# Optimization experiments

Hardware: AMD Instinct MI355X
Metric: run time of the kernel (lower is better)

## Reference

```python
import jax, jax.numpy as jnp
import numpy as np

B, T, D, H = 4, 2048, 1024, 16
Dh = D // H


def setup_inputs() -> dict:
    key = jax.random.key(0)
    ks = jax.random.split(key, 10)
    s = 0.02  # init scale for weights
    return {
        "x": jax.random.normal(ks[0], (B, T, D), jnp.float32),
        "gates": jax.random.uniform(ks[1], (B, H), jnp.float32),
        "Wq": jax.random.normal(ks[2], (D, D), jnp.float32) * s,
        "bq": jnp.zeros((D,), jnp.float32),
        "Wk": jax.random.normal(ks[3], (D, D), jnp.float32) * s,
        "bk": jnp.zeros((D,), jnp.float32),
        "Wv": jax.random.normal(ks[4], (D, D), jnp.float32) * s,
        "bv": jnp.zeros((D,), jnp.float32),
        "Wo": jax.random.normal(ks[5], (D, D), jnp.float32) * s,
        "bo": jnp.zeros((D,), jnp.float32),
    }


def reference(x, gates, Wq, bq, Wk, bk, Wv, bv, Wo, bo):
    # x: [B,T,D], gates: [B,H]. torch Linear is y = x @ W.T + b.
    b, t, d = x.shape
    h = gates.shape[1]
    dh = d // h
    q = (x @ Wq.T + bq).reshape(b, t, h, dh)
    k = (x @ Wk.T + bk).reshape(b, t, h, dh)
    v = (x @ Wv.T + bv).reshape(b, t, h, dh)
    scores = jnp.einsum('bthd,bshd->bhts', q, k) / jnp.sqrt(jnp.float32(dh))
    A = jax.nn.softmax(scores, axis=-1)
    A = A * gates[:, :, None, None]  # post-softmax per-head gate
    z = jnp.einsum('bhts,bshd->bthd', A, v).reshape(b, t, d)
    out = z @ Wo.T + bo
    return out, A
```

## Files before the change

kernel.cpp:

```cpp
#include <hip/hip_runtime.h>

#define BB 4
#define TT 2048
#define DD 1024
#define HH 16
#define DHH 64

using half8  = __attribute__((ext_vector_type(8))) _Float16;
using half4v = __attribute__((ext_vector_type(4))) _Float16;
using f32x4  = __attribute__((ext_vector_type(4))) float;

#define EXP2C 0.18033688011112042f

__device__ __forceinline__ float fexp2(float x) {
#if __has_builtin(__builtin_amdgcn_exp2f)
  return __builtin_amdgcn_exp2f(x);
#else
  return exp2f(x);
#endif
}

__device__ __forceinline__ void gload_lds16(const _Float16* g, _Float16* l) {
  __builtin_amdgcn_global_load_lds((const __attribute__((address_space(1))) void*)g,
                                   (__attribute__((address_space(3))) void*)l, 16, 0, 0);
}

__global__ void cvt_all(const float* __restrict__ x,
                        const float* __restrict__ wq, const float* __restrict__ wk,
                        const float* __restrict__ wv, const float* __restrict__ wo,
                        _Float16* __restrict__ xh,
                        _Float16* __restrict__ wqh, _Float16* __restrict__ wkh,
                        _Float16* __restrict__ wvh, _Float16* __restrict__ woh) {
  const float* s; _Float16* d; int n8, b0, nb;
  int b = blockIdx.x;
  if (b < 512) { s = x; d = xh; n8 = BB * TT * DD / 8; b0 = b; nb = 512; }
  else {
    int wsel = (b - 512) >> 6;
    b0 = (b - 512) & 63; nb = 64; n8 = DD * DD / 8;
    s = wsel == 0 ? wq : wsel == 1 ? wk : wsel == 2 ? wv : wo;
    d = wsel == 0 ? wqh : wsel == 1 ? wkh : wsel == 2 ? wvh : woh;
  }
  for (int i = b0 * 256 + threadIdx.x; i < n8; i += nb * 256) {
    const float4* p = (const float4*)(s + (size_t)i * 8);
    float4 a = p[0], bb = p[1];
    half8 h;
    h[0] = (_Float16)a.x; h[1] = (_Float16)a.y; h[2] = (_Float16)a.z; h[3] = (_Float16)a.w;
    h[4] = (_Float16)bb.x; h[5] = (_Float16)bb.y; h[6] = (_Float16)bb.z; h[7] = (_Float16)bb.w;
    *(half8*)(d + (size_t)i * 8) = h;
  }
}

#define GEMM_STAGE(K0, BSEL)                                                        \
  _Pragma("unroll") for (int it = 0; it < 4; ++it) {                                \
    int chunk = tid + it * 256;                                                     \
    int r = chunk >> 3, pb = chunk & 7, lb = pb ^ (r & 7);                          \
    gload_lds16(A + (size_t)(row0 + r) * K + (K0) * 64 + lb * 8, As[BSEL] + chunk * 8);  \
    gload_lds16(Bw + (size_t)(col0 + r) * K + (K0) * 64 + lb * 8, Bs[BSEL] + chunk * 8); \
  }

__global__ __launch_bounds__(256, 2) void gemm_qkv(const _Float16* __restrict__ A,
                                                   const _Float16* __restrict__ Wqh,
                                                   const _Float16* __restrict__ Wkh,
                                                   const _Float16* __restrict__ Wvh,
                                                   const float* __restrict__ bq,
                                                   const float* __restrict__ bk,
                                                   const float* __restrict__ bv,
                                                   _Float16* __restrict__ qh,
                                                   _Float16* __restrict__ kh,
                                                   _Float16* __restrict__ vTh) {
  constexpr int K = 1024;
  __shared__ _Float16 As[2][128 * 64];
  __shared__ _Float16 Bs[2][128 * 64];
  const int tid = threadIdx.x;
  const int l = tid & 63, w = tid >> 6;
  const int wm = w >> 1, wn = w & 1;
  const int lg = l >> 4, lr16 = l & 15;
  const int wsel = (int)blockIdx.y >> 3;
  const _Float16* Bw = wsel == 0 ? Wqh : wsel == 1 ? Wkh : Wvh;
  const float* bias = wsel == 0 ? bq : wsel == 1 ? bk : bv;
  const int row0 = blockIdx.x * 128, col0 = ((int)blockIdx.y & 7) * 128;

  f32x4 acc[4][4];
#pragma unroll
  for (int i = 0; i < 4; ++i)
#pragma unroll
    for (int j = 0; j < 4; ++j) acc[i][j] = (f32x4)0.0f;

  GEMM_STAGE(0, 0);
  int cur = 0;
  for (int k0 = 0; k0 < 16; ++k0) {
    __syncthreads();
    if (k0 < 15) GEMM_STAGE(k0 + 1, cur ^ 1);
#pragma unroll
    for (int kb = 0; kb < 2; ++kb) {
      half8 a[4], b[4];
#pragma unroll
      for (int f = 0; f < 4; ++f) {
        int ar = wm * 64 + f * 16 + lr16;
        a[f] = *(const half8*)(As[cur] + ar * 64 + ((kb * 4 + lg) ^ (ar & 7)) * 8);
        int br = wn * 64 + f * 16 + lr16;
        b[f] = *(const half8*)(Bs[cur] + br * 64 + ((kb * 4 + lg) ^ (br & 7)) * 8);
      }
#pragma unroll
      for (int i = 0; i < 4; ++i)
#pragma unroll
        for (int j = 0; j < 4; ++j)
          acc[i][j] = __builtin_amdgcn_mfma_f32_16x16x32_f16(a[i], b[j], acc[i][j], 0, 0, 0);
    }
    cur ^= 1;
  }

#pragma unroll
  for (int fi = 0; fi < 4; ++fi) {
#pragma unroll
    for (int fj = 0; fj < 4; ++fj) {
      int gi0 = row0 + wm * 64 + fi * 16 + lg * 4;
      int gj = col0 + wn * 64 + fj * 16 + lr16;
      float bj = bias[gj];
      int b = gi0 >> 11, t0 = gi0 & 2047;
      int h = gj >> 6, dh = gj & 63;
      if (wsel < 2) {
        _Float16* O = wsel ? kh : qh;
#pragma unroll
        for (int r = 0; r < 4; ++r)
          O[(((size_t)(b * HH + h) * TT + (t0 + r)) << 6) + dh] = (_Float16)(acc[fi][fj][r] + bj);
      } else {
        half4v tmp;
#pragma unroll
        for (int r = 0; r < 4; ++r) tmp[r] = (_Float16)(acc[fi][fj][r] + bj);
        *(half4v*)(vTh + (((size_t)(b * HH + h) * DHH + dh) * TT + t0)) = tmp;
      }
    }
  }
}

__global__ __launch_bounds__(256, 2) void gemm_out(const _Float16* __restrict__ A,
                                                   const _Float16* __restrict__ Bw,
                                                   const float* __restrict__ bias,
                                                   float* __restrict__ Cout) {
  constexpr int K = 1024;
  __shared__ _Float16 As[2][128 * 64];
  __shared__ _Float16 Bs[2][128 * 64];
  const int tid = threadIdx.x;
  const int l = tid & 63, w = tid >> 6;
  const int wm = w >> 1, wn = w & 1;
  const int lg = l >> 4, lr16 = l & 15;
  const int row0 = blockIdx.x * 128, col0 = blockIdx.y * 128;

  f32x4 acc[4][4];
#pragma unroll
  for (int i = 0; i < 4; ++i)
#pragma unroll
    for (int j = 0; j < 4; ++j) acc[i][j] = (f32x4)0.0f;

  GEMM_STAGE(0, 0);
  int cur = 0;
  for (int k0 = 0; k0 < 16; ++k0) {
    __syncthreads();
    if (k0 < 15) GEMM_STAGE(k0 + 1, cur ^ 1);
#pragma unroll
    for (int kb = 0; kb < 2; ++kb) {
      half8 a[4], b[4];
#pragma unroll
      for (int f = 0; f < 4; ++f) {
        int ar = wm * 64 + f * 16 + lr16;
        a[f] = *(const half8*)(As[cur] + ar * 64 + ((kb * 4 + lg) ^ (ar & 7)) * 8);
        int br = wn * 64 + f * 16 + lr16;
        b[f] = *(const half8*)(Bs[cur] + br * 64 + ((kb * 4 + lg) ^ (br & 7)) * 8);
      }
#pragma unroll
      for (int i = 0; i < 4; ++i)
#pragma unroll
        for (int j = 0; j < 4; ++j)
          acc[i][j] = __builtin_amdgcn_mfma_f32_16x16x32_f16(a[i], b[j], acc[i][j], 0, 0, 0);
    }
    cur ^= 1;
  }

#pragma unroll
  for (int fi = 0; fi < 4; ++fi) {
#pragma unroll
    for (int fj = 0; fj < 4; ++fj) {
      int gi0 = row0 + wm * 64 + fi * 16 + lg * 4;
      int gj = col0 + wn * 64 + fj * 16 + lr16;
      float bj = bias[gj];
#pragma unroll
      for (int r = 0; r < 4; ++r)
        __builtin_nontemporal_store(acc[fi][fj][r] + bj, &Cout[(size_t)(gi0 + r) * DD + gj]);
    }
  }
}

__global__ __launch_bounds__(512, 2) void attn_kernel(const _Float16* __restrict__ qh,
                                                      const _Float16* __restrict__ kh,
                                                      const _Float16* __restrict__ vTh,
                                                      const float* __restrict__ gates,
                                                      float* __restrict__ Aout,
                                                      _Float16* __restrict__ zh) {
  __shared__ _Float16 Qs[128 * 64];
  __shared__ _Float16 Ks[2][64 * 64];
  __shared__ _Float16 Vs[2][64 * 64];
  __shared__ _Float16 Ps[128 * 64];
  const int tid = threadIdx.x;
  const int l = tid & 63, w = tid >> 6;
  const int lg = l >> 4, lr16 = l & 15;
  const int wr0 = w * 16;
  const int blk = ((int)blockIdx.x & 7) * 128 + ((int)blockIdx.x >> 3);
  const int rt = blk & 15, bh = blk >> 4;
  const _Float16* Qp = qh + (size_t)bh * TT * DHH + (size_t)rt * 128 * DHH;
  const _Float16* Kp = kh + (size_t)bh * TT * DHH;
  const _Float16* Vp = vTh + (size_t)bh * DHH * TT;
  float* Ap = Aout + (size_t)bh * TT * TT + (size_t)rt * 128 * TT;
  const float gate = gates[bh];

#pragma unroll
  for (int it = 0; it < 2; ++it) {
    int chunk = tid + it * 512;
    int r = chunk >> 3, pb = chunk & 7, lb = pb ^ (r & 7);
    gload_lds16(Qp + (size_t)r * DHH + lb * 8, Qs + chunk * 8);
  }

#define STAGE_K(CT, BSEL) {                                                   \
    int chunk = tid; int r = chunk >> 3, pb = chunk & 7, lb = pb ^ (r & 7);   \
    gload_lds16(Kp + (size_t)((CT) * 64 + r) * DHH + lb * 8, Ks[BSEL] + chunk * 8); }
#define STAGE_V(CT, BSEL) {                                                   \
    int chunk = tid; int r = chunk >> 3, pb = chunk & 7, lb = pb ^ (r & 7);   \
    gload_lds16(Vp + (size_t)r * TT + (CT) * 64 + lb * 8, Vs[BSEL] + chunk * 8); }

  STAGE_K(0, 0);
  float rs = 0.f;
  int cur = 0;
  for (int ct = 0; ct < 32; ++ct) {
    __syncthreads();
    if (ct < 31) STAGE_K(ct + 1, cur ^ 1);
    f32x4 s[4];
#pragma unroll
    for (int j = 0; j < 4; ++j) s[j] = (f32x4)0.0f;
    __builtin_amdgcn_s_setprio(1);
#pragma unroll
    for (int kb = 0; kb < 2; ++kb) {
      int qr = wr0 + lr16;
      half8 aQ = *(const half8*)(Qs + qr * 64 + (((kb * 4 + lg) ^ (qr & 7)) * 8));
      half8 bK[4];
#pragma unroll
      for (int fc = 0; fc < 4; ++fc) {
        int kr = fc * 16 + lr16;
        bK[fc] = *(const half8*)(Ks[cur] + kr * 64 + (((kb * 4 + lg) ^ (kr & 7)) * 8));
      }
#pragma unroll
      for (int fc = 0; fc < 4; ++fc)
        s[fc] = __builtin_amdgcn_mfma_f32_16x16x32_f16(bK[fc], aQ, s[fc], 0, 0, 0);
    }
    __builtin_amdgcn_s_setprio(0);
#pragma unroll
    for (int fc = 0; fc < 4; ++fc)
#pragma unroll
      for (int r = 0; r < 4; ++r) rs += fexp2(s[fc][r] * EXP2C);
    cur ^= 1;
  }

  {
    rs += __shfl_xor(rs, 16, 64);
    rs += __shfl_xor(rs, 32, 64);
  }
  const float inv = gate / rs;

  f32x4 z[4];
#pragma unroll
  for (int j = 0; j < 4; ++j) z[j] = (f32x4)0.0f;
  STAGE_K(0, 0);
  STAGE_V(0, 0);
  asm volatile("s_waitcnt vmcnt(0)\n\ts_barrier" ::: "memory");
  cur = 0;
  for (int ct = 0; ct < 32; ++ct) {
    if (ct < 31) {
      STAGE_K(ct + 1, cur ^ 1);
      STAGE_V(ct + 1, cur ^ 1);
    }
    __builtin_amdgcn_sched_barrier(0);
    f32x4 s[4];
#pragma unroll
    for (int j = 0; j < 4; ++j) s[j] = (f32x4)0.0f;
    __builtin_amdgcn_s_setprio(1);
#pragma unroll
    for (int kb = 0; kb < 2; ++kb) {
      int qr = wr0 + lr16;
      half8 aQ = *(const half8*)(Qs + qr * 64 + (((kb * 4 + lg) ^ (qr & 7)) * 8));
      half8 bK[4];
#pragma unroll
      for (int fc = 0; fc < 4; ++fc) {
        int kr = fc * 16 + lr16;
        bK[fc] = *(const half8*)(Ks[cur] + kr * 64 + (((kb * 4 + lg) ^ (kr & 7)) * 8));
      }
#pragma unroll
      for (int fc = 0; fc < 4; ++fc)
        s[fc] = __builtin_amdgcn_mfma_f32_16x16x32_f16(bK[fc], aQ, s[fc], 0, 0, 0);
    }
    __builtin_amdgcn_s_setprio(0);
    const int q = wr0 + lr16;
#pragma unroll
    for (int fc = 0; fc < 4; ++fc) {
      f32x4 o;
      half4v ph;
#pragma unroll
      for (int r = 0; r < 4; ++r) {
        float av = fexp2(s[fc][r] * EXP2C) * inv;
        o[r] = av;
        ph[r] = (_Float16)av;
      }
      __builtin_nontemporal_store(o, (f32x4*)(Ap + (size_t)q * TT + ct * 64 + fc * 16 + lg * 4));
      int g8 = fc * 2 + (lg >> 1);
      *(half4v*)(Ps + q * 64 + ((g8 ^ (q & 7)) * 8) + (lg & 1) * 4) = ph;
    }
    __builtin_amdgcn_s_setprio(1);
#pragma unroll
    for (int kb = 0; kb < 2; ++kb) {
      int pr = wr0 + lr16;
      half8 aP = *(const half8*)(Ps + pr * 64 + (((kb * 4 + lg) ^ (pr & 7)) * 8));
      half8 bV[4];
#pragma unroll
      for (int fc = 0; fc < 4; ++fc) {
        int vr = fc * 16 + lr16;
        bV[fc] = *(const half8*)(Vs[cur] + vr * 64 + (((kb * 4 + lg) ^ (vr & 7)) * 8));
      }
#pragma unroll
      for (int fc = 0; fc < 4; ++fc)
        z[fc] = __builtin_amdgcn_mfma_f32_16x16x32_f16(aP, bV[fc], z[fc], 0, 0, 0);
    }
    __builtin_amdgcn_s_setprio(0);
    if (ct < 31) {
      asm volatile("s_waitcnt vmcnt(4) lgkmcnt(0)\n\ts_barrier" ::: "memory");
    }
    cur ^= 1;
  }

  const int b = bh >> 4, h = bh & 15;
  _Float16* zp = zh + ((size_t)b * TT + (size_t)rt * 128) * DD + h * 64;
  const int rbase = wr0 + lg * 4;
#pragma unroll
  for (int fc = 0; fc < 4; ++fc) {
    int d = fc * 16 + lr16;
#pragma unroll
    for (int r = 0; r < 4; ++r) zp[(size_t)(rbase + r) * DD + d] = (_Float16)z[fc][r];
  }
}

extern "C" void kernel_launch(void* const* d_in, const int* in_sizes, int n_in,
                              void* d_out, int out_size, void* d_ws, size_t ws_size,
                              hipStream_t stream) {
  const float* x     = (const float*)d_in[0];
  const float* gates = (const float*)d_in[1];
  const float* Wq    = (const float*)d_in[2];
  const float* bq    = (const float*)d_in[3];
  const float* Wk    = (const float*)d_in[4];
  const float* bk    = (const float*)d_in[5];
  const float* Wv    = (const float*)d_in[6];
  const float* bv    = (const float*)d_in[7];
  const float* Wo    = (const float*)d_in[8];
  const float* bo    = (const float*)d_in[9];

  float* out  = (float*)d_out;
  float* Aout = out + (size_t)BB * TT * DD;

  char* ws = (char*)d_ws;
  _Float16* xh  = (_Float16*)(ws);
  _Float16* Wqh = (_Float16*)(ws + (16ull << 20));
  _Float16* Wkh = (_Float16*)(ws + (18ull << 20));
  _Float16* Wvh = (_Float16*)(ws + (20ull << 20));
  _Float16* Woh = (_Float16*)(ws + (22ull << 20));
  _Float16* qh  = (_Float16*)(ws + (24ull << 20));
  _Float16* kh  = (_Float16*)(ws + (40ull << 20));
  _Float16* vTh = (_Float16*)(ws + (56ull << 20));
  _Float16* zh  = xh;

  cvt_all<<<768, 256, 0, stream>>>(x, Wq, Wk, Wv, Wo, xh, Wqh, Wkh, Wvh, Woh);

  gemm_qkv<<<dim3(BB * TT / 128, 24), 256, 0, stream>>>(xh, Wqh, Wkh, Wvh, bq, bk, bv,
                                                        qh, kh, vTh);

  attn_kernel<<<BB * HH * (TT / 128), 512, 0, stream>>>(qh, kh, vTh, gates, Aout, zh);

  gemm_out<<<dim3(BB * TT / 128, DD / 128), 256, 0, stream>>>(zh, Woh, bo, out);
}
```

Measured before the change: 459.3 us.

## Drop LDS staging in attention, accumulate PV in first pass, direct global loads

The attention kernel no longer stages Q/K/V through shared memory. Each wave loads its operands straight from global memory into registers, and the LDS buffers and barriers are removed. The P·V product is now accumulated in the first pass using unnormalized exponentials and scaled by the gated inverse row sum at the end, so the second pass only recomputes scores to write A. Occupancy hints rise to 4 blocks and nontemporal stores become plain stores. This saves synchronisation and LDS traffic, but in exchange K/V are fetched repeatedly per wave from L2/global and the loads use narrower, less coalesced access patterns.

```diff
diff --git a/kernel.cpp b/kernel.cpp
--- a/kernel.cpp
+++ b/kernel.cpp
@@ -186,21 +186,17 @@
       float bj = bias[gj];
 #pragma unroll
       for (int r = 0; r < 4; ++r)
-        __builtin_nontemporal_store(acc[fi][fj][r] + bj, &Cout[(size_t)(gi0 + r) * DD + gj]);
-    }
-  }
-}
-
-__global__ __launch_bounds__(512, 2) void attn_kernel(const _Float16* __restrict__ qh,
+        Cout[(size_t)(gi0 + r) * DD + gj] = acc[fi][fj][r] + bj;
+    }
+  }
+}
+
+__global__ __launch_bounds__(512, 4) void attn_kernel(const _Float16* __restrict__ qh,
                                                       const _Float16* __restrict__ kh,
                                                       const _Float16* __restrict__ vTh,
                                                       const float* __restrict__ gates,
                                                       float* __restrict__ Aout,
                                                       _Float16* __restrict__ zh) {
-  __shared__ _Float16 Qs[128 * 64];
-  __shared__ _Float16 Ks[2][64 * 64];
-  __shared__ _Float16 Vs[2][64 * 64];
-  __shared__ _Float16 Ps[128 * 64];
   const int tid = threadIdx.x;
   const int l = tid & 63, w = tid >> 6;
   const int lg = l >> 4, lr16 = l & 15;
@@ -213,136 +209,86 @@
   float* Ap = Aout + (size_t)bh * TT * TT + (size_t)rt * 128 * TT;
   const float gate = gates[bh];
 
-#pragma unroll
-  for (int it = 0; it < 2; ++it) {
-    int chunk = tid + it * 512;
-    int r = chunk >> 3, pb = chunk & 7, lb = pb ^ (r & 7);
-    gload_lds16(Qp + (size_t)r * DHH + lb * 8, Qs + chunk * 8);
-  }
-
-#define STAGE_K(CT, BSEL) {                                                   \
-    int chunk = tid; int r = chunk >> 3, pb = chunk & 7, lb = pb ^ (r & 7);   \
-    gload_lds16(Kp + (size_t)((CT) * 64 + r) * DHH + lb * 8, Ks[BSEL] + chunk * 8); }
-#define STAGE_V(CT, BSEL) {                                                   \
-    int chunk = tid; int r = chunk >> 3, pb = chunk & 7, lb = pb ^ (r & 7);   \
-    gload_lds16(Vp + (size_t)r * TT + (CT) * 64 + lb * 8, Vs[BSEL] + chunk * 8); }
-
-  STAGE_K(0, 0);
+  const int qrow = wr0 + lr16;
+  const half8 aQ0 = *(const half8*)(Qp + (size_t)qrow * DHH + lg * 8);
+  const half8 aQ1 = *(const half8*)(Qp + (size_t)qrow * DHH + (4 + lg) * 8);
+
   float rs = 0.f;
-  int cur = 0;
+  f32x4 z[4];
+#pragma unroll
+  for (int j = 0; j < 4; ++j) z[j] = (f32x4)0.0f;
+
   for (int ct = 0; ct < 32; ++ct) {
-    __syncthreads();
-    if (ct < 31) STAGE_K(ct + 1, cur ^ 1);
+    const _Float16* Kt = Kp + (size_t)ct * 64 * DHH;
+    const _Float16* Vt = Vp + (size_t)ct * 64;
     f32x4 s[4];
 #pragma unroll
     for (int j = 0; j < 4; ++j) s[j] = (f32x4)0.0f;
-    __builtin_amdgcn_s_setprio(1);
 #pragma unroll
     for (int kb = 0; kb < 2; ++kb) {
-      int qr = wr0 + lr16;
-      half8 aQ = *(const half8*)(Qs + qr * 64 + (((kb * 4 + lg) ^ (qr & 7)) * 8));
-      half8 bK[4];
+      half8 aQ = kb ? aQ1 : aQ0;
 #pragma unroll
       for (int fc = 0; fc < 4; ++fc) {
-        int kr = fc * 16 + lr16;
-        bK[fc] = *(const half8*)(Ks[cur] + kr * 64 + (((kb * 4 + lg) ^ (kr & 7)) * 8));
-      }
-#pragma unroll
-      for (int fc = 0; fc < 4; ++fc)
-        s[fc] = __builtin_amdgcn_mfma_f32_16x16x32_f16(bK[fc], aQ, s[fc], 0, 0, 0);
-    }
-    __builtin_amdgcn_s_setprio(0);
-#pragma unroll
-    for (int fc = 0; fc < 4; ++fc)
-#pragma unroll
-      for (int r = 0; r < 4; ++r) rs += fexp2(s[fc][r] * EXP2C);
-    cur ^= 1;
-  }
-
-  {
-    rs += __shfl_xor(rs, 16, 64);
-    rs += __shfl_xor(rs, 32, 64);
-  }
+        half8 bK = *(const half8*)(Kt + (size_t)(fc * 16 + lr16) * DHH + (kb * 4 + lg) * 8);
+        s[fc] = __builtin_amdgcn_mfma_f32_16x16x32_f16(bK, aQ, s[fc], 0, 0, 0);
+      }
+    }
+#pragma unroll
+    for (int fc = 0; fc < 4; ++fc) {
+      half4v ph;
+#pragma unroll
+      for (int r = 0; r < 4; ++r) {
+        float p = fexp2(s[fc][r] * EXP2C);
+        rs += p;
+        ph[r] = (_Float16)p;
+      }
+#pragma unroll
+      for (int fcol = 0; fcol < 4; ++fcol) {
+        half4v bV = *(const half4v*)(Vt + (size_t)(fcol * 16 + lr16) * TT + fc * 16 + lg * 4);
+        z[fcol] = __builtin_amdgcn_mfma_f32_16x16x16f16(ph, bV, z[fcol], 0, 0, 0);
+      }
+    }
+  }
+
+  rs += __shfl_xor(rs, 16, 64);
+  rs += __shfl_xor(rs, 32, 64);
   const float inv = gate / rs;
-
-  f32x4 z[4];
-#pragma unroll
-  for (int j = 0; j < 4; ++j) z[j] = (f32x4)0.0f;
-  STAGE_K(0, 0);
-  STAGE_V(0, 0);
-  asm volatile("s_waitcnt vmcnt(0)\n\ts_barrier" ::: "memory");
-  cur = 0;
+  f32x4 inv4;
+#pragma unroll
+  for (int r = 0; r < 4; ++r) inv4[r] = __shfl(inv, lg * 4 + r, 64);
+
   for (int ct = 0; ct < 32; ++ct) {
-    if (ct < 31) {
-      STAGE_K(ct + 1, cur ^ 1);
-      STAGE_V(ct + 1, cur ^ 1);
-    }
-    __builtin_amdgcn_sched_barrier(0);
+    const _Float16* Kt = Kp + (size_t)ct * 64 * DHH;
     f32x4 s[4];
 #pragma unroll
     for (int j = 0; j < 4; ++j) s[j] = (f32x4)0.0f;
-    __builtin_amdgcn_s_setprio(1);
 #pragma unroll
     for (int kb = 0; kb < 2; ++kb) {
-      int qr = wr0 + lr16;
-      half8 aQ = *(const half8*)(Qs + qr * 64 + (((kb * 4 + lg) ^ (qr & 7)) * 8));
-      half8 bK[4];
+      half8 aQ = kb ? aQ1 : aQ0;
 #pragma unroll
       for (int fc = 0; fc < 4; ++fc) {
-        int kr = fc * 16 + lr16;
-        bK[fc] = *(const half8*)(Ks[cur] + kr * 64 + (((kb * 4 + lg) ^ (kr & 7)) * 8));
-      }
-#pragma unroll
-      for (int fc = 0; fc < 4; ++fc)
-        s[fc] = __builtin_amdgcn_mfma_f32_16x16x32_f16(bK[fc], aQ, s[fc], 0, 0, 0);
-    }
-    __builtin_amdgcn_s_setprio(0);
-    const int q = wr0 + lr16;
+        half8 bK = *(const half8*)(Kt + (size_t)(fc * 16 + lr16) * DHH + (kb * 4 + lg) * 8);
+        s[fc] = __builtin_amdgcn_mfma_f32_16x16x32_f16(bK, aQ, s[fc], 0, 0, 0);
+      }
+    }
 #pragma unroll
     for (int fc = 0; fc < 4; ++fc) {
       f32x4 o;
-      half4v ph;
-#pragma unroll
-      for (int r = 0; r < 4; ++r) {
-        float av = fexp2(s[fc][r] * EXP2C) * inv;
-        o[r] = av;
-        ph[r] = (_Float16)av;
-      }
-      __builtin_nontemporal_store(o, (f32x4*)(Ap + (size_t)q * TT + ct * 64 + fc * 16 + lg * 4));
-      int g8 = fc * 2 + (lg >> 1);
-      *(half4v*)(Ps + q * 64 + ((g8 ^ (q & 7)) * 8) + (lg & 1) * 4) = ph;
-    }
-    __builtin_amdgcn_s_setprio(1);
-#pragma unroll
-    for (int kb = 0; kb < 2; ++kb) {
-      int pr = wr0 + lr16;
-      half8 aP = *(const half8*)(Ps + pr * 64 + (((kb * 4 + lg) ^ (pr & 7)) * 8));
-      half8 bV[4];
-#pragma unroll
-      for (int fc = 0; fc < 4; ++fc) {
-        int vr = fc * 16 + lr16;
-        bV[fc] = *(const half8*)(Vs[cur] + vr * 64 + (((kb * 4 + lg) ^ (vr & 7)) * 8));
-      }
-#pragma unroll
-      for (int fc = 0; fc < 4; ++fc)
-        z[fc] = __builtin_amdgcn_mfma_f32_16x16x32_f16(aP, bV[fc], z[fc], 0, 0, 0);
-    }
-    __builtin_amdgcn_s_setprio(0);
-    if (ct < 31) {
-      asm volatile("s_waitcnt vmcnt(4) lgkmcnt(0)\n\ts_barrier" ::: "memory");
-    }
-    cur ^= 1;
+#pragma unroll
+      for (int r = 0; r < 4; ++r) o[r] = fexp2(s[fc][r] * EXP2C) * inv;
+      *(f32x4*)(Ap + (size_t)qrow * TT + ct * 64 + fc * 16 + lg * 4) = o;
+    }
   }
 
   const int b = bh >> 4, h = bh & 15;
-  _Float16* zp = zh + ((size_t)b * TT + (size_t)rt * 128) * DD + h * 64;
-  const int rbase = wr0 + lg * 4;
-#pragma unroll
-  for (int fc = 0; fc < 4; ++fc) {
-    int d = fc * 16 + lr16;
-#pragma unroll
-    for (int r = 0; r < 4; ++r) zp[(size_t)(rbase + r) * DD + d] = (_Float16)z[fc][r];
-  }
+#pragma unroll
+  for (int fcol = 0; fcol < 4; ++fcol)
+#pragma unroll
+    for (int j = 0; j < 4; ++j) {
+      int q = rt * 128 + wr0 + lg * 4 + j;
+      zh[((size_t)(b * TT + q)) * DD + h * 64 + fcol * 16 + lr16] =
+          (_Float16)(z[fcol][j] * inv4[j]);
+    }
 }
 
 extern "C" void kernel_launch(void* const* d_in, const int* in_sizes, int n_in,
```

Measured after the change: 1.062 ms. 131% more time.

## Keep Q and P in registers and stage attention output through LDS

Applied to the files above, without the earlier changes.

The attention kernel now loads each wave's Q fragments into registers once, using the K buffer as temporary scratch, and drops the Qs array. The softmax probabilities are fed straight from registers into 16x16x16 f16 MFMAs, with no round trip through a shared P buffer. The fp32 A tile is written to a per-wave swizzled LDS buffer and then read back so that each group of 16 lanes stores a full contiguous 256-byte row, instead of scattered 16-byte pieces across rows. This targets global-store coalescing for the very large A output and removes LDS traffic for Q and P. In exchange it adds extra LDS writes and reads for A, uses the smaller-K MFMA shape, and replaces the nontemporal stores with plain ones.

```diff
diff --git a/kernel.cpp b/kernel.cpp
--- a/kernel.cpp
+++ b/kernel.cpp
@@ -197,10 +197,9 @@
                                                       const float* __restrict__ gates,
                                                       float* __restrict__ Aout,
                                                       _Float16* __restrict__ zh) {
-  __shared__ _Float16 Qs[128 * 64];
   __shared__ _Float16 Ks[2][64 * 64];
   __shared__ _Float16 Vs[2][64 * 64];
-  __shared__ _Float16 Ps[128 * 64];
+  __shared__ float Sf[8][16 * 64];
   const int tid = threadIdx.x;
   const int l = tid & 63, w = tid >> 6;
   const int lg = l >> 4, lr16 = l & 15;
@@ -212,20 +211,30 @@
   const _Float16* Vp = vTh + (size_t)bh * DHH * TT;
   float* Ap = Aout + (size_t)bh * TT * TT + (size_t)rt * 128 * TT;
   const float gate = gates[bh];
-
-#pragma unroll
-  for (int it = 0; it < 2; ++it) {
-    int chunk = tid + it * 512;
-    int r = chunk >> 3, pb = chunk & 7, lb = pb ^ (r & 7);
-    gload_lds16(Qp + (size_t)r * DHH + lb * 8, Qs + chunk * 8);
-  }
+  float* Sfw = Sf[w];
+
+  {
+    _Float16* Qscratch = &Ks[0][0];
+#pragma unroll
+    for (int it = 0; it < 2; ++it) {
+      int chunk = tid + it * 512;
+      int r = chunk >> 3, pb = chunk & 7, lb = pb ^ (r & 7);
+      gload_lds16(Qp + (size_t)r * DHH + lb * 8, Qscratch + chunk * 8);
+    }
+  }
+  asm volatile("s_waitcnt vmcnt(0)" ::: "memory");
+  __syncthreads();
+  const int qr = wr0 + lr16;
+  const half8 aQ0 = *(const half8*)(&Ks[0][0] + qr * 64 + ((lg ^ (qr & 7)) * 8));
+  const half8 aQ1 = *(const half8*)(&Ks[0][0] + qr * 64 + (((4 + lg) ^ (qr & 7)) * 8));
+  __syncthreads();
 
 #define STAGE_K(CT, BSEL) {                                                   \
-    int chunk = tid; int r = chunk >> 3, pb = chunk & 7, lb = pb ^ (r & 7);   \
-    gload_lds16(Kp + (size_t)((CT) * 64 + r) * DHH + lb * 8, Ks[BSEL] + chunk * 8); }
+    int r = tid >> 3, pb = tid & 7, lb = pb ^ (r & 7);                        \
+    gload_lds16(Kp + (size_t)((CT) * 64 + r) * DHH + lb * 8, Ks[BSEL] + tid * 8); }
 #define STAGE_V(CT, BSEL) {                                                   \
-    int chunk = tid; int r = chunk >> 3, pb = chunk & 7, lb = pb ^ (r & 7);   \
-    gload_lds16(Vp + (size_t)r * TT + (CT) * 64 + lb * 8, Vs[BSEL] + chunk * 8); }
+    int r = tid >> 3, pb = tid & 7, lb = pb ^ (r & 7);                        \
+    gload_lds16(Vp + (size_t)r * TT + (CT) * 64 + lb * 8, Vs[BSEL] + tid * 8); }
 
   STAGE_K(0, 0);
   float rs = 0.f;
@@ -239,8 +248,7 @@
     __builtin_amdgcn_s_setprio(1);
 #pragma unroll
     for (int kb = 0; kb < 2; ++kb) {
-      int qr = wr0 + lr16;
-      half8 aQ = *(const half8*)(Qs + qr * 64 + (((kb * 4 + lg) ^ (qr & 7)) * 8));
+      half8 aQ = kb ? aQ1 : aQ0;
       half8 bK[4];
 #pragma unroll
       for (int fc = 0; fc < 4; ++fc) {
@@ -259,10 +267,8 @@
     cur ^= 1;
   }
 
-  {
-    rs += __shfl_xor(rs, 16, 64);
-    rs += __shfl_xor(rs, 32, 64);
-  }
+  rs += __shfl_xor(rs, 16, 64);
+  rs += __shfl_xor(rs, 32, 64);
   const float inv = gate / rs;
 
   f32x4 z[4];
@@ -284,8 +290,7 @@
     __builtin_amdgcn_s_setprio(1);
 #pragma unroll
     for (int kb = 0; kb < 2; ++kb) {
-      int qr = wr0 + lr16;
-      half8 aQ = *(const half8*)(Qs + qr * 64 + (((kb * 4 + lg) ^ (qr & 7)) * 8));
+      half8 aQ = kb ? aQ1 : aQ0;
       half8 bK[4];
 #pragma unroll
       for (int fc = 0; fc < 4; ++fc) {
@@ -297,37 +302,42 @@
         s[fc] = __builtin_amdgcn_mfma_f32_16x16x32_f16(bK[fc], aQ, s[fc], 0, 0, 0);
     }
     __builtin_amdgcn_s_setprio(0);
-    const int q = wr0 + lr16;
+
+    half4v ph4[4];
 #pragma unroll
     for (int fc = 0; fc < 4; ++fc) {
       f32x4 o;
-      half4v ph;
 #pragma unroll
       for (int r = 0; r < 4; ++r) {
         float av = fexp2(s[fc][r] * EXP2C) * inv;
         o[r] = av;
-        ph[r] = (_Float16)av;
-      }
-      __builtin_nontemporal_store(o, (f32x4*)(Ap + (size_t)q * TT + ct * 64 + fc * 16 + lg * 4));
-      int g8 = fc * 2 + (lg >> 1);
-      *(half4v*)(Ps + q * 64 + ((g8 ^ (q & 7)) * 8) + (lg & 1) * 4) = ph;
-    }
+        ph4[fc][r] = (_Float16)av;
+      }
+      int gw = fc * 4 + lg;
+      *(f32x4*)(Sfw + lr16 * 64 + ((gw ^ lr16) * 4)) = o;
+    }
+
     __builtin_amdgcn_s_setprio(1);
 #pragma unroll
-    for (int kb = 0; kb < 2; ++kb) {
-      int pr = wr0 + lr16;
-      half8 aP = *(const half8*)(Ps + pr * 64 + (((kb * 4 + lg) ^ (pr & 7)) * 8));
-      half8 bV[4];
-#pragma unroll
-      for (int fc = 0; fc < 4; ++fc) {
-        int vr = fc * 16 + lr16;
-        bV[fc] = *(const half8*)(Vs[cur] + vr * 64 + (((kb * 4 + lg) ^ (vr & 7)) * 8));
-      }
-#pragma unroll
-      for (int fc = 0; fc < 4; ++fc)
-        z[fc] = __builtin_amdgcn_mfma_f32_16x16x32_f16(aP, bV[fc], z[fc], 0, 0, 0);
+    for (int fc = 0; fc < 4; ++fc) {
+#pragma unroll
+      for (int fcol = 0; fcol < 4; ++fcol) {
+        int vr = fcol * 16 + lr16;
+        int g8 = fc * 2 + (lg >> 1);
+        half4v bV = *(const half4v*)(Vs[cur] + vr * 64 + (((g8 ^ (vr & 7)) * 8)) + (lg & 1) * 4);
+        z[fcol] = __builtin_amdgcn_mfma_f32_16x16x16f16(ph4[fc], bV, z[fcol], 0, 0, 0);
+      }
     }
     __builtin_amdgcn_s_setprio(0);
+
+#pragma unroll
+    for (int j = 0; j < 4; ++j) {
+      int r = (l >> 4) + j * 4;
+      int g = l & 15;
+      f32x4 ov = *(const f32x4*)(Sfw + r * 64 + ((g ^ r) * 4));
+      *(f32x4*)(Ap + (size_t)(wr0 + r) * TT + ct * 64 + g * 4) = ov;
+    }
+
     if (ct < 31) {
       asm volatile("s_waitcnt vmcnt(4) lgkmcnt(0)\n\ts_barrier" ::: "memory");
     }
@@ -338,10 +348,10 @@
   _Float16* zp = zh + ((size_t)b * TT + (size_t)rt * 128) * DD + h * 64;
   const int rbase = wr0 + lg * 4;
 #pragma unroll
-  for (int fc = 0; fc < 4; ++fc) {
-    int d = fc * 16 + lr16;
-#pragma unroll
-    for (int r = 0; r < 4; ++r) zp[(size_t)(rbase + r) * DD + d] = (_Float16)z[fc][r];
+  for (int fcol = 0; fcol < 4; ++fcol) {
+    int d = fcol * 16 + lr16;
+#pragma unroll
+    for (int j = 0; j < 4; ++j) zp[(size_t)(rbase + j) * DD + d] = (_Float16)z[fcol][j];
   }
 }
 
```

Result: slower. 470.8 us (+2.5%).
